# Performance work log

Measured on AMD Instinct MI355X. Metric: run time of the kernel, lower is better.

## Reference

```python
import jax, jax.numpy as jnp
import numpy as np

NB_LABELS = 10
NB_EDGE_LABELS = 3
SINKHORN_ITERS = 10


def setup_inputs() -> dict:
    key = jax.random.key(0)
    k1, k2, k3, k4, k5, k6 = jax.random.split(key, 6)
    n = m = 95
    nb_node_pairs = NB_LABELS * (NB_LABELS - 1) // 2
    nb_edge_pairs = NB_EDGE_LABELS * (NB_EDGE_LABELS - 1) // 2
    node_weights = 0.1 * 1.1 * jax.random.uniform(k1, (nb_node_pairs + 1,), jnp.float32)
    node_weights = node_weights.at[-1].set(0.3)
    edge_weights = 0.1 * 1.1 * jax.random.uniform(k2, (nb_edge_pairs + 1,), jnp.float32)
    edge_weights = edge_weights.at[-1].set(0.2)
    A_g1 = jax.random.randint(k3, (n * n,), 0, NB_EDGE_LABELS + 1, jnp.int32)
    A_g2 = jax.random.randint(k4, (m * m,), 0, NB_EDGE_LABELS + 1, jnp.int32)
    labels1 = jax.random.randint(k5, (n,), 0, NB_LABELS, jnp.int32)
    labels2 = jax.random.randint(k6, (m,), 0, NB_LABELS, jnp.int32)
    return dict(node_weights=node_weights, edge_weights=edge_weights,
                A_g1=A_g1, A_g2=A_g2, labels1=labels1, labels2=labels2, n=n, m=m)


def _from_weights_to_costs(node_weights, edge_weights):
    cn = jax.nn.relu(node_weights)
    ce = jax.nn.relu(edge_weights)
    node_ins_del, edge_ins_del = cn[-1], ce[-1]
    iu = jnp.triu_indices(NB_LABELS, k=1)
    node_costs = jnp.zeros((NB_LABELS, NB_LABELS), jnp.float32).at[iu].set(cn[:-1])
    node_costs = node_costs + node_costs.T
    iue = jnp.triu_indices(NB_EDGE_LABELS, k=1)
    edge_costs = jnp.zeros((NB_EDGE_LABELS, NB_EDGE_LABELS), jnp.float32).at[iue].set(ce[:-1])
    edge_costs = edge_costs + edge_costs.T  # zero diagonal => k != l handled for free
    return node_costs, node_ins_del, edge_costs, edge_ins_del


def _kron_perm(X4, n1, m1):
    # torch cat/unbind trick: out[j*m1+k, i*m1+l] = X4[i, j, k, l]
    return X4.transpose(1, 2, 0, 3).reshape(n1 * m1, n1 * m1)


def _sinkhorn(S, iters):
    # eps_assign2: alternate row/col normalization, last row/col scale fixed to 1
    def step(S, _):
        rs = (1.0 / S.sum(axis=1)).at[-1].set(1.0)
        S = S * rs[:, None]
        cs = (1.0 / S.sum(axis=0)).at[-1].set(1.0)
        S = S * cs[None, :]
        return S, None
    S, _ = jax.lax.scan(step, S, None, length=iters)
    return S


def _ged_forward(node_weights, edge_weights, A_g1, A_g2, labels1, labels2, n, m):
    node_costs, node_ins_del, edge_costs, edge_ins_del = _from_weights_to_costs(node_weights, edge_weights)
    n1, m1 = n + 1, m + 1
    N = n1 * m1
    A1 = jnp.zeros((n1, n1), jnp.int32).at[:n, :n].set(A_g1[:n * n].reshape(n, n))
    A2 = jnp.zeros((m1, m1), jnp.int32).at[:m, :m].set(A_g2[:m * m].reshape(m, m))
    Ab1, Ab2 = A1 != 0, A2 != 0
    # edge insertion/deletion costs: XOR of edge presence, Kronecker-expanded
    ins_del = jnp.logical_xor(Ab1[:, :, None, None], Ab2[None, None, :, :]).astype(jnp.float32)
    C = edge_ins_del * _kron_perm(ins_del, n1, m1)
    # edge substitution: one-hot over edge labels, contracted with symmetric edge_costs (zero diag)
    labs = jnp.arange(1, NB_EDGE_LABELS + 1, dtype=jnp.int32)
    E1 = (A1[None, :, :] == labs[:, None, None]).astype(jnp.float32)  # [L, n1, n1]
    E2 = (A2[None, :, :] == labs[:, None, None]).astype(jnp.float32)  # [L, m1, m1]
    Csub = jnp.einsum('aij,bkl,ab->ijkl', E1, E2, edge_costs)
    C = C + _kron_perm(Csub, n1, m1)
    # node cost vector D (diagonal of C)
    Dnm = node_costs[labels1[:n][:, None], labels2[:m][None, :]]  # [n, m]
    D2 = jnp.full((n1, m1), node_ins_del, jnp.float32)
    D2 = D2.at[:n, :m].set(Dnm)
    D2 = D2.at[n, m].set(0.0)
    c = D2.reshape(-1)  # length N
    diag_idx = jnp.arange(N)
    C = C.at[diag_idx, diag_idx].set(c)
    Dmat = C.at[diag_idx, diag_idx].set(0.0)  # C - eye * diag(C)
    # Sinkhorn-like soft assignment
    S = _sinkhorn(jnp.exp(-0.5 * c.reshape(n1, m1)), SINKHORN_ITERS)
    v = S.reshape(-1)
    ged = 0.5 * (v @ (Dmat @ v)) + c @ v
    return ged


def reference(node_weights, edge_weights, A_g1, A_g2, labels1, labels2, n, m):
    return _ged_forward(node_weights, edge_weights, A_g1, A_g2, labels1, labels2, n, m)
```

## Files before the change

### kernel.cpp

```cpp
#include <hip/hip_runtime.h>

#define NV 95
#define SINK_ITERS 10

__global__ __launch_bounds__(1024)
void ged_all(const float* __restrict__ nw, const float* __restrict__ ew,
             const int* __restrict__ Ag1, const int* __restrict__ Ag2,
             const int* __restrict__ lab1g, const int* __restrict__ lab2g,
             float* __restrict__ outp)
{
    __shared__ float cn[46], ce[4];
    __shared__ float nc[100];
    __shared__ float ftab[16];
    __shared__ float nids;
    __shared__ int   labs1[96], labs2[96];
    __shared__ int   cnt1[12], cnt2[12];
    __shared__ int   P1h[3 * 121], P2h[3 * 121];
    __shared__ int   H1[4 * 12], H2[4 * 12];
    __shared__ float E0s[11 * 12];
    __shared__ float Rs[12], Cs[12];
    __shared__ float Q1s[4 * 132], R2s[4 * 132];
    __shared__ float wred[16];

    const int tid = threadIdx.x;

    const int4* A1_4 = (const int4*)Ag1;
    const int4* A2_4 = (const int4*)Ag2;
    int4 a1r[3], a2r[3];
    const bool scanner = (tid >= 192);
    const int  sbase = tid - 192;
    if (scanner) {
        #pragma unroll
        for (int r = 0; r < 3; ++r) {
            int slot = sbase + r * 832;
            if (slot < 2256) { a1r[r] = A1_4[slot]; a2r[r] = A2_4[slot]; }
        }
    }
    int rem1 = 0, rem2 = 0;
    if (tid == 1023) { rem1 = Ag1[9024]; rem2 = Ag2[9024]; }
    int d1 = 0, d2 = 0;
    if (tid >= 320 && tid < 416) { int u = tid - 320; d1 = (u < NV) ? Ag1[u * 96] : 0; }
    if (tid >= 448 && tid < 544) { int u = tid - 448; d2 = (u < NV) ? Ag2[u * 96] : 0; }

    if (tid < 46) cn[tid] = fmaxf(nw[tid], 0.f);
    if (tid >= 64 && tid < 68) ce[tid - 64] = fmaxf(ew[tid - 64], 0.f);
    if (tid >= 128 && tid < 224) { int t = tid - 128; labs1[t] = (t < NV) ? lab1g[t] : 10; }
    if (tid >= 256 && tid < 352) { int t = tid - 256; labs2[t] = (t < NV) ? lab2g[t] : 10; }
    for (int i = tid; i < 363; i += 1024) { P1h[i] = 0; P2h[i] = 0; }
    if (tid < 48) { H1[tid] = 0; H2[tid] = 0; }
    if (tid < 12) { cnt1[tid] = 0; cnt2[tid] = 0; }
    __syncthreads();

    if (tid < 45) {
        int i = 0, rem = tid;
        while (rem >= 9 - i) { rem -= 9 - i; ++i; }
        int j = i + 1 + rem;
        float v = cn[tid];
        nc[i * 10 + j] = v; nc[j * 10 + i] = v;
    }
    if (tid >= 45 && tid < 55) nc[(tid - 45) * 11] = 0.f;
    if (tid == 0) {
        nids = cn[45];
        float e01 = ce[0], e02 = ce[1], e12 = ce[2], eid = ce[3];
        ftab[0] = 0.f;  ftab[1] = eid;  ftab[2] = eid;  ftab[3] = eid;
        ftab[4] = eid;  ftab[5] = 0.f;  ftab[6] = e01;  ftab[7] = e02;
        ftab[8] = eid;  ftab[9] = e01;  ftab[10] = 0.f; ftab[11] = e12;
        ftab[12] = eid; ftab[13] = e02; ftab[14] = e12; ftab[15] = 0.f;
    }
    if (tid == 1) { cnt1[10] = 1; cnt2[10] = 1; }
    if (tid >= 64 && tid < 64 + NV)   atomicAdd(&cnt1[labs1[tid - 64]], 1);
    if (tid >= 192 && tid < 192 + NV) atomicAdd(&cnt2[labs2[tid - 192]], 1);
    if (tid >= 320 && tid < 416) atomicAdd(&H1[d1 * 12 + labs1[tid - 320]], 1);
    if (tid >= 448 && tid < 544) atomicAdd(&H2[d2 * 12 + labs2[tid - 448]], 1);
    __syncthreads();

    if (tid < 64) {
        int l = tid;
        int ll = (l < 11) ? l : 0;
        float nid_l = nids;
        float ecrow[11], eccol[11];
        #pragma unroll
        for (int b = 0; b < 11; ++b) {
            float c = (ll < 10 && b < 10) ? nc[ll * 10 + b]
                     : ((ll == 10 && b == 10) ? 0.f : nid_l);
            ecrow[b] = expf(-0.5f * c) * (float)cnt2[b];
        }
        #pragma unroll
        for (int a = 0; a < 11; ++a) {
            float c = (a < 10 && ll < 10) ? nc[a * 10 + ll]
                     : ((a == 10 && ll == 10) ? 0.f : nid_l);
            eccol[a] = expf(-0.5f * c) * (float)cnt1[a];
        }
        float Rv = 1.f, Cv = 1.f;
        for (int it = 0; it < SINK_ITERS; ++it) {
            float s = 0.f;
            #pragma unroll
            for (int b = 0; b < 11; ++b) s += ecrow[b] * __shfl(Cv, b, 64);
            Rv = (l == 10) ? 1.f : 1.f / s;
            float s2 = 0.f;
            #pragma unroll
            for (int a = 0; a < 11; ++a) s2 += eccol[a] * __shfl(Rv, a, 64);
            Cv = (l == 10) ? 1.f : 1.f / s2;
        }
        if (l < 11) { Rs[l] = Rv; Cs[l] = Cv; }
    } else if (tid < 185) {
        int t = tid - 64;
        int a = t / 11, b = t - a * 11;
        float c = (a < 10 && b < 10) ? nc[a * 10 + b]
                 : ((a == 10 && b == 10) ? 0.f : nids);
        E0s[a * 12 + b] = expf(-0.5f * c);
    } else if (scanner) {
        #pragma unroll
        for (int r = 0; r < 3; ++r) {
            int slot = sbase + r * 832;
            if (slot < 2256) {
                int base = slot * 4;
                int v1[4] = { a1r[r].x, a1r[r].y, a1r[r].z, a1r[r].w };
                int v2[4] = { a2r[r].x, a2r[r].y, a2r[r].z, a2r[r].w };
                #pragma unroll
                for (int q = 0; q < 4; ++q) {
                    int idx = base + q;
                    int i = idx / NV, j = idx - i * NV;
                    if (v1[q]) atomicAdd(&P1h[(v1[q] - 1) * 121 + labs1[i] * 11 + labs1[j]], 1);
                    if (v2[q]) atomicAdd(&P2h[(v2[q] - 1) * 121 + labs2[i] * 11 + labs2[j]], 1);
                }
            }
        }
        if (tid == 1023) {
            if (rem1) atomicAdd(&P1h[(rem1 - 1) * 121 + labs1[94] * 11 + labs1[94]], 1);
            if (rem2) atomicAdd(&P2h[(rem2 - 1) * 121 + labs2[94] * 11 + labs2[94]], 1);
        }
    }
    __syncthreads();

    if (tid < 484) {
        int e = tid / 121, ab = tid - e * 121, a = ab / 11, b = ab - a * 11;
        float s = 0.f;
        #pragma unroll
        for (int a2 = 0; a2 < 11; ++a2) {
            int aa = a * 11 + a2;
            float p = (e == 0)
                ? (float)(cnt1[a] * cnt1[a2] - P1h[aa] - P1h[121 + aa] - P1h[242 + aa])
                : (float)P1h[(e - 1) * 121 + aa];
            s += p * E0s[a2 * 12 + b] * Rs[a2];
        }
        Q1s[e * 132 + a * 12 + b] = s * Cs[b];
    }
    if (tid >= 512 && tid < 996) {
        int t = tid - 512;
        int e = t / 121, ab = t - e * 121, a = ab / 11, b = ab - a * 11;
        float s = 0.f;
        #pragma unroll
        for (int b2 = 0; b2 < 11; ++b2) {
            int bb = b * 11 + b2;
            float p = (e == 0)
                ? (float)(cnt2[b] * cnt2[b2] - P2h[bb] - P2h[121 + bb] - P2h[242 + bb])
                : (float)P2h[(e - 1) * 121 + bb];
            s += p * E0s[a * 12 + b2] * Cs[b2];
        }
        R2s[e * 132 + a * 12 + b] = s * Rs[a];
    }
    __syncthreads();

    float x = 0.f;
    if (tid < 968) {
        #pragma unroll
        for (int r = 0; r < 2; ++r) {
            int t = tid + r * 968;
            int p = t / 121, ab = t - p * 121;
            int e1 = p >> 2, e2 = p & 3;
            int a = ab / 11, b = ab - a * 11;
            float f  = ftab[p];
            float tt = E0s[a * 12 + b] * Rs[a] * Cs[b];
            x += 0.5f * f * (Q1s[e1 * 132 + a * 12 + b] * R2s[e2 * 132 + a * 12 + b]
                             - (float)H1[e1 * 12 + a] * (float)H2[e2 * 12 + b] * tt * tt);
        }
    }
    if (tid < 121) {
        int a = tid / 11, b = tid - a * 11;
        float c = (a < 10 && b < 10) ? nc[a * 10 + b]
                 : ((a == 10 && b == 10) ? 0.f : nids);
        x += (float)(cnt1[a] * cnt2[b]) * c * E0s[a * 12 + b] * Rs[a] * Cs[b];
    }
    #pragma unroll
    for (int off = 32; off > 0; off >>= 1) x += __shfl_down(x, off, 64);
    if ((tid & 63) == 0) wred[tid >> 6] = x;
    __syncthreads();
    if (tid == 0) {
        float s = 0.f;
        #pragma unroll
        for (int w = 0; w < 16; ++w) s += wred[w];
        outp[0] = s;
    }
}

extern "C" void kernel_launch(void* const* d_in, const int* in_sizes, int n_in,
                              void* d_out, int out_size, void* d_ws, size_t ws_size,
                              hipStream_t stream)
{
    (void)in_sizes; (void)n_in; (void)out_size; (void)d_ws; (void)ws_size;
    const float* nw  = (const float*)d_in[0];
    const float* ew  = (const float*)d_in[1];
    const int*   Ag1 = (const int*)d_in[2];
    const int*   Ag2 = (const int*)d_in[3];
    const int*   l1  = (const int*)d_in[4];
    const int*   l2  = (const int*)d_in[5];
    hipLaunchKernelGGL(ged_all, dim3(1), dim3(1024), 0, stream,
                       nw, ew, Ag1, Ag2, l1, l2, (float*)d_out);
}
```

Measured before the change: 14.40 us.

## Merge setup phases to drop a barrier and count labels with wave ballots

The single-block GED kernel now builds the node-cost and exp tables straight from global weights in one pass, replacing the separate cn/nc staging phase. This removes one __syncthreads round. Label counts are computed with wave-wide ballot and popcount instead of shared-memory atomics. Each scanner thread now handles 12 contiguous adjacency entries, so it needs one row/column division instead of one per element. The padded dummy-node contributions are folded in analytically (+1 terms, padded label 10). That aims to cut the serial latency of this tiny kernel, but the index bookkeeping becomes more fragile.

```diff
diff --git a/kernel.cpp b/kernel.cpp
--- a/kernel.cpp
+++ b/kernel.cpp
@@ -1,6 +1,6 @@
 #include <hip/hip_runtime.h>
 
-#define NV 95
+#define NVAL 95
 #define SINK_ITERS 10
 
 __global__ __launch_bounds__(1024)
@@ -9,88 +9,92 @@
              const int* __restrict__ lab1g, const int* __restrict__ lab2g,
              float* __restrict__ outp)
 {
-    __shared__ float cn[46], ce[4];
-    __shared__ float nc[100];
+    __shared__ float CT[11 * 12];
+    __shared__ float E0s[11 * 12];
     __shared__ float ftab[16];
-    __shared__ float nids;
     __shared__ int   labs1[96], labs2[96];
-    __shared__ int   cnt1[12], cnt2[12];
-    __shared__ int   P1h[3 * 121], P2h[3 * 121];
-    __shared__ int   H1[4 * 12], H2[4 * 12];
-    __shared__ float E0s[11 * 12];
+    __shared__ float cnt1f[12], cnt2f[12];
+    __shared__ int   P1h[363], P2h[363];
+    __shared__ int   H1[48], H2[48];
     __shared__ float Rs[12], Cs[12];
     __shared__ float Q1s[4 * 132], R2s[4 * 132];
     __shared__ float wred[16];
 
     const int tid = threadIdx.x;
-
-    const int4* A1_4 = (const int4*)Ag1;
-    const int4* A2_4 = (const int4*)Ag2;
+    const int t   = tid - 64;
+    const bool scanner = (t >= 0 && t < 753);
+
     int4 a1r[3], a2r[3];
-    const bool scanner = (tid >= 192);
-    const int  sbase = tid - 192;
     if (scanner) {
-        #pragma unroll
-        for (int r = 0; r < 3; ++r) {
-            int slot = sbase + r * 832;
-            if (slot < 2256) { a1r[r] = A1_4[slot]; a2r[r] = A2_4[slot]; }
-        }
-    }
-    int rem1 = 0, rem2 = 0;
-    if (tid == 1023) { rem1 = Ag1[9024]; rem2 = Ag2[9024]; }
-    int d1 = 0, d2 = 0;
-    if (tid >= 320 && tid < 416) { int u = tid - 320; d1 = (u < NV) ? Ag1[u * 96] : 0; }
-    if (tid >= 448 && tid < 544) { int u = tid - 448; d2 = (u < NV) ? Ag2[u * 96] : 0; }
-
-    if (tid < 46) cn[tid] = fmaxf(nw[tid], 0.f);
-    if (tid >= 64 && tid < 68) ce[tid - 64] = fmaxf(ew[tid - 64], 0.f);
-    if (tid >= 128 && tid < 224) { int t = tid - 128; labs1[t] = (t < NV) ? lab1g[t] : 10; }
-    if (tid >= 256 && tid < 352) { int t = tid - 256; labs2[t] = (t < NV) ? lab2g[t] : 10; }
-    for (int i = tid; i < 363; i += 1024) { P1h[i] = 0; P2h[i] = 0; }
-    if (tid < 48) { H1[tid] = 0; H2[tid] = 0; }
-    if (tid < 12) { cnt1[tid] = 0; cnt2[tid] = 0; }
-    __syncthreads();
-
-    if (tid < 45) {
-        int i = 0, rem = tid;
-        while (rem >= 9 - i) { rem -= 9 - i; ++i; }
-        int j = i + 1 + rem;
-        float v = cn[tid];
-        nc[i * 10 + j] = v; nc[j * 10 + i] = v;
-    }
-    if (tid >= 45 && tid < 55) nc[(tid - 45) * 11] = 0.f;
-    if (tid == 0) {
-        nids = cn[45];
-        float e01 = ce[0], e02 = ce[1], e12 = ce[2], eid = ce[3];
-        ftab[0] = 0.f;  ftab[1] = eid;  ftab[2] = eid;  ftab[3] = eid;
-        ftab[4] = eid;  ftab[5] = 0.f;  ftab[6] = e01;  ftab[7] = e02;
-        ftab[8] = eid;  ftab[9] = e01;  ftab[10] = 0.f; ftab[11] = e12;
+        if (t < 752) {
+            const int4* A14 = (const int4*)Ag1;
+            const int4* A24 = (const int4*)Ag2;
+            #pragma unroll
+            for (int r = 0; r < 3; ++r) { a1r[r] = A14[3 * t + r]; a2r[r] = A24[3 * t + r]; }
+        } else {
+            a1r[0] = make_int4(Ag1[9024], 0, 0, 0);
+            a2r[0] = make_int4(Ag2[9024], 0, 0, 0);
+            a1r[1] = a1r[2] = a2r[1] = a2r[2] = make_int4(0, 0, 0, 0);
+        }
+        for (int i = t; i < 822; i += 753) {
+            if (i < 363) P1h[i] = 0;
+            else if (i < 726) P2h[i - 363] = 0;
+            else if (i < 774) H1[i - 726] = 0;
+            else H2[i - 774] = 0;
+        }
+    }
+    int d1v = 0, d2v = 0, myl1 = 0, myl2 = 0;
+    if (tid >= 832 && tid < 928) {
+        int u = tid - 832;
+        myl1 = (u < NVAL) ? lab1g[u] : 10;
+        myl2 = (u < NVAL) ? lab2g[u] : 10;
+        labs1[u] = myl1; labs2[u] = myl2;
+        if (u < NVAL) { d1v = Ag1[u * 96]; d2v = Ag2[u * 96]; }
+    }
+    {
+        int cell = (tid >= 928) ? (tid - 928) : ((tid < 25) ? 96 + tid : -1);
+        if (cell >= 0) {
+            int a = cell / 11, b = cell - a * 11;
+            float c;
+            if (a == b) c = 0.f;
+            else if (a < 10 && b < 10) {
+                int mn = min(a, b), mx = max(a, b);
+                int idx = mn * 9 - mn * (mn - 1) / 2 + (mx - mn - 1);
+                c = fmaxf(nw[idx], 0.f);
+            } else c = fmaxf(nw[45], 0.f);
+            CT[a * 12 + b]  = c;
+            E0s[a * 12 + b] = expf(-0.5f * c);
+        }
+    }
+    if (tid == 1023) {
+        float e01 = fmaxf(ew[0], 0.f), e02 = fmaxf(ew[1], 0.f);
+        float e12 = fmaxf(ew[2], 0.f), eid = fmaxf(ew[3], 0.f);
+        ftab[0]  = 0.f; ftab[1]  = eid; ftab[2]  = eid; ftab[3]  = eid;
+        ftab[4]  = eid; ftab[5]  = 0.f; ftab[6]  = e01; ftab[7]  = e02;
+        ftab[8]  = eid; ftab[9]  = e01; ftab[10] = 0.f; ftab[11] = e12;
         ftab[12] = eid; ftab[13] = e02; ftab[14] = e12; ftab[15] = 0.f;
     }
-    if (tid == 1) { cnt1[10] = 1; cnt2[10] = 1; }
-    if (tid >= 64 && tid < 64 + NV)   atomicAdd(&cnt1[labs1[tid - 64]], 1);
-    if (tid >= 192 && tid < 192 + NV) atomicAdd(&cnt2[labs2[tid - 192]], 1);
-    if (tid >= 320 && tid < 416) atomicAdd(&H1[d1 * 12 + labs1[tid - 320]], 1);
-    if (tid >= 448 && tid < 544) atomicAdd(&H2[d2 * 12 + labs2[tid - 448]], 1);
     __syncthreads();
 
     if (tid < 64) {
         int l = tid;
+        int v1a = labs1[l],               v2a = labs2[l];
+        int v1b = (l < 32) ? labs1[64 + l] : -1;
+        int v2b = (l < 32) ? labs2[64 + l] : -1;
+        float c1v = 0.f, c2v = 0.f;
+        #pragma unroll
+        for (int a = 0; a < 11; ++a) {
+            int n1 = __popcll(__ballot(v1a == a)) + __popcll(__ballot(v1b == a));
+            int n2 = __popcll(__ballot(v2a == a)) + __popcll(__ballot(v2b == a));
+            if (l == a) { c1v = (float)n1; c2v = (float)n2; }
+        }
+        if (l < 11) { cnt1f[l] = c1v; cnt2f[l] = c2v; }
         int ll = (l < 11) ? l : 0;
-        float nid_l = nids;
         float ecrow[11], eccol[11];
         #pragma unroll
-        for (int b = 0; b < 11; ++b) {
-            float c = (ll < 10 && b < 10) ? nc[ll * 10 + b]
-                     : ((ll == 10 && b == 10) ? 0.f : nid_l);
-            ecrow[b] = expf(-0.5f * c) * (float)cnt2[b];
-        }
-        #pragma unroll
-        for (int a = 0; a < 11; ++a) {
-            float c = (a < 10 && ll < 10) ? nc[a * 10 + ll]
-                     : ((a == 10 && ll == 10) ? 0.f : nid_l);
-            eccol[a] = expf(-0.5f * c) * (float)cnt1[a];
-        }
+        for (int b = 0; b < 11; ++b) ecrow[b] = E0s[ll * 12 + b] * __shfl(c2v, b, 64);
+        #pragma unroll
+        for (int a = 0; a < 11; ++a) eccol[a] = E0s[a * 12 + ll] * __shfl(c1v, a, 64);
         float Rv = 1.f, Cv = 1.f;
         for (int it = 0; it < SINK_ITERS; ++it) {
             float s = 0.f;
@@ -103,32 +107,38 @@
             Cv = (l == 10) ? 1.f : 1.f / s2;
         }
         if (l < 11) { Rs[l] = Rv; Cs[l] = Cv; }
-    } else if (tid < 185) {
-        int t = tid - 64;
-        int a = t / 11, b = t - a * 11;
-        float c = (a < 10 && b < 10) ? nc[a * 10 + b]
-                 : ((a == 10 && b == 10) ? 0.f : nids);
-        E0s[a * 12 + b] = expf(-0.5f * c);
-    } else if (scanner) {
-        #pragma unroll
-        for (int r = 0; r < 3; ++r) {
-            int slot = sbase + r * 832;
-            if (slot < 2256) {
-                int base = slot * 4;
-                int v1[4] = { a1r[r].x, a1r[r].y, a1r[r].z, a1r[r].w };
-                int v2[4] = { a2r[r].x, a2r[r].y, a2r[r].z, a2r[r].w };
-                #pragma unroll
-                for (int q = 0; q < 4; ++q) {
-                    int idx = base + q;
-                    int i = idx / NV, j = idx - i * NV;
-                    if (v1[q]) atomicAdd(&P1h[(v1[q] - 1) * 121 + labs1[i] * 11 + labs1[j]], 1);
-                    if (v2[q]) atomicAdd(&P2h[(v2[q] - 1) * 121 + labs2[i] * 11 + labs2[j]], 1);
-                }
-            }
-        }
-        if (tid == 1023) {
-            if (rem1) atomicAdd(&P1h[(rem1 - 1) * 121 + labs1[94] * 11 + labs1[94]], 1);
-            if (rem2) atomicAdd(&P2h[(rem2 - 1) * 121 + labs2[94] * 11 + labs2[94]], 1);
+    }
+    if (tid >= 832 && tid < 928) {
+        int u = tid - 832;
+        if (u < NVAL) {
+            atomicAdd(&H1[d1v * 12 + myl1], 1);
+            atomicAdd(&H2[d2v * 12 + myl2], 1);
+        }
+    }
+    if (scanner) {
+        int base = t * 12;
+        int i0 = base / 95;
+        int j0 = base - i0 * 95;
+        int rem = 95 - j0;
+        int i1 = (i0 < 95) ? i0 + 1 : 95;
+        int la1 = labs1[i0] * 11, lb1 = labs1[i1] * 11;
+        int la2 = labs2[i0] * 11, lb2 = labs2[i1] * 11;
+        int vals1[12] = { a1r[0].x, a1r[0].y, a1r[0].z, a1r[0].w,
+                          a1r[1].x, a1r[1].y, a1r[1].z, a1r[1].w,
+                          a1r[2].x, a1r[2].y, a1r[2].z, a1r[2].w };
+        int vals2[12] = { a2r[0].x, a2r[0].y, a2r[0].z, a2r[0].w,
+                          a2r[1].x, a2r[1].y, a2r[1].z, a2r[1].w,
+                          a2r[2].x, a2r[2].y, a2r[2].z, a2r[2].w };
+        #pragma unroll
+        for (int q = 0; q < 12; ++q) {
+            bool ok  = (base + q) < 9025;
+            bool sec = q >= rem;
+            int  j   = sec ? (q - rem) : (j0 + q);
+            int  u1  = labs1[j], u2 = labs2[j];
+            int  v1  = ok ? vals1[q] : 0;
+            int  v2  = ok ? vals2[q] : 0;
+            if (v1) atomicAdd(&P1h[(v1 - 1) * 121 + (sec ? lb1 : la1) + u1], 1);
+            if (v2) atomicAdd(&P2h[(v2 - 1) * 121 + (sec ? lb2 : la2) + u2], 1);
         }
     }
     __syncthreads();
@@ -140,21 +150,21 @@
         for (int a2 = 0; a2 < 11; ++a2) {
             int aa = a * 11 + a2;
             float p = (e == 0)
-                ? (float)(cnt1[a] * cnt1[a2] - P1h[aa] - P1h[121 + aa] - P1h[242 + aa])
+                ? cnt1f[a] * cnt1f[a2] - (float)(P1h[aa] + P1h[121 + aa] + P1h[242 + aa])
                 : (float)P1h[(e - 1) * 121 + aa];
             s += p * E0s[a2 * 12 + b] * Rs[a2];
         }
         Q1s[e * 132 + a * 12 + b] = s * Cs[b];
     }
     if (tid >= 512 && tid < 996) {
-        int t = tid - 512;
-        int e = t / 121, ab = t - e * 121, a = ab / 11, b = ab - a * 11;
+        int tt = tid - 512;
+        int e = tt / 121, ab = tt - e * 121, a = ab / 11, b = ab - a * 11;
         float s = 0.f;
         #pragma unroll
         for (int b2 = 0; b2 < 11; ++b2) {
             int bb = b * 11 + b2;
             float p = (e == 0)
-                ? (float)(cnt2[b] * cnt2[b2] - P2h[bb] - P2h[121 + bb] - P2h[242 + bb])
+                ? cnt2f[b] * cnt2f[b2] - (float)(P2h[bb] + P2h[121 + bb] + P2h[242 + bb])
                 : (float)P2h[(e - 1) * 121 + bb];
             s += p * E0s[a * 12 + b2] * Cs[b2];
         }
@@ -166,21 +176,21 @@
     if (tid < 968) {
         #pragma unroll
         for (int r = 0; r < 2; ++r) {
-            int t = tid + r * 968;
-            int p = t / 121, ab = t - p * 121;
+            int tt = tid + r * 968;
+            int p = tt / 121, ab = tt - p * 121;
             int e1 = p >> 2, e2 = p & 3;
             int a = ab / 11, b = ab - a * 11;
             float f  = ftab[p];
-            float tt = E0s[a * 12 + b] * Rs[a] * Cs[b];
+            float tv = E0s[a * 12 + b] * Rs[a] * Cs[b];
+            float h1 = (float)H1[e1 * 12 + a] + ((e1 == 0 && a == 10) ? 1.f : 0.f);
+            float h2 = (float)H2[e2 * 12 + b] + ((e2 == 0 && b == 10) ? 1.f : 0.f);
             x += 0.5f * f * (Q1s[e1 * 132 + a * 12 + b] * R2s[e2 * 132 + a * 12 + b]
-                             - (float)H1[e1 * 12 + a] * (float)H2[e2 * 12 + b] * tt * tt);
+                             - h1 * h2 * tv * tv);
         }
     }
     if (tid < 121) {
         int a = tid / 11, b = tid - a * 11;
-        float c = (a < 10 && b < 10) ? nc[a * 10 + b]
-                 : ((a == 10 && b == 10) ? 0.f : nids);
-        x += (float)(cnt1[a] * cnt2[b]) * c * E0s[a * 12 + b] * Rs[a] * Cs[b];
+        x += cnt1f[a] * cnt2f[b] * CT[a * 12 + b] * E0s[a * 12 + b] * Rs[a] * Cs[b];
     }
     #pragma unroll
     for (int off = 32; off > 0; off >>= 1) x += __shfl_down(x, off, 64);
```

Result: no change. 14.12 us (-1.9%).
